# Kernel tuning notes

Measured on AMD Instinct MI355X. Metric: run time of the kernel, lower is better.

The kernel has to match this reference:

```python
import jax, jax.numpy as jnp
import numpy as np

N = 50000
E = 800000
D_IN = 128
D_HID = 512
D_OUT = 128
BN_EPS = 1e-5


def setup_inputs() -> dict:
    key = jax.random.key(0)
    ks = jax.random.split(key, 12)
    inp = {}
    inp["v"] = jax.random.normal(ks[0], (N, D_IN), dtype=jnp.float32)
    inp["src"] = jax.random.randint(ks[1], (E,), 0, N, dtype=jnp.int32)
    inp["dst"] = jax.random.randint(ks[2], (E,), 0, N, dtype=jnp.int32)
    inp["edge_weight"] = jax.random.uniform(ks[3], (E,), dtype=jnp.float32)
    # learned parameters
    inp["epsilon"] = jnp.zeros((1, 1), dtype=jnp.float32)  # nn.Parameter([[0.0]])
    s1 = 1.0 / np.sqrt(D_IN)
    s2 = 1.0 / np.sqrt(D_HID)
    inp["W1"] = jax.random.uniform(ks[4], (D_IN, D_HID), minval=-s1, maxval=s1, dtype=jnp.float32)
    inp["b1"] = jax.random.uniform(ks[5], (D_HID,), minval=-s1, maxval=s1, dtype=jnp.float32)
    inp["gamma1"] = jnp.ones((D_HID,), dtype=jnp.float32)
    inp["beta1"] = jnp.zeros((D_HID,), dtype=jnp.float32)
    inp["W2"] = jax.random.uniform(ks[6], (D_HID, D_OUT), minval=-s2, maxval=s2, dtype=jnp.float32)
    inp["b2"] = jax.random.uniform(ks[7], (D_OUT,), minval=-s2, maxval=s2, dtype=jnp.float32)
    inp["gamma2"] = jnp.ones((D_OUT,), dtype=jnp.float32)
    inp["beta2"] = jnp.zeros((D_OUT,), dtype=jnp.float32)
    return inp


def _batchnorm(x, gamma, beta):
    # training-mode BN: batch mean / biased variance over the node axis
    mean = jnp.mean(x, axis=0)
    var = jnp.mean(jnp.square(x - mean), axis=0)
    return gamma * (x - mean) * jax.lax.rsqrt(var + BN_EPS) + beta


def reference(v, src, dst, edge_weight, epsilon, W1, b1, gamma1, beta1, W2, b2, gamma2, beta2):
    n = v.shape[0]
    # sparse.mm(a, v): out[dst] += w * v[src]
    msgs = v[src] * edge_weight[:, None]               # [E, D_IN]
    v_agg = jax.ops.segment_sum(msgs, dst, num_segments=n)  # [N, D_IN]
    v_agg = v_agg + epsilon * v                        # epsilon residual
    h = jax.nn.relu(_batchnorm(v_agg @ W1 + b1, gamma1, beta1))
    out = jax.nn.relu(_batchnorm(h @ W2 + b2, gamma2, beta2))
    return out
```

## Files before the change

kernel.cpp:

```cpp
#include <hip/hip_runtime.h>

#define N_NODES 50000
#define E_EDGES 800000
#define D_INF   128
#define D_HIDF  512
#define D_OUTF  128
#define SCAN_NB ((N_NODES + 255) / 256)
#define MBLKS   ((N_NODES + 255) / 256)
#define G2BLKS  ((N_NODES + 63) / 64)
#define EQ      (E_EDGES / 4)

typedef unsigned short u16;
typedef __attribute__((ext_vector_type(8))) short short8;
typedef __attribute__((ext_vector_type(4))) float floatx4;

__device__ __forceinline__ u16 f2bf(float f) {
    union { float f; unsigned u; } v; v.f = f;
    unsigned r = (v.u + 0x7fffu + ((v.u >> 16) & 1u)) >> 16;
    return (u16)r;
}
__device__ __forceinline__ float bf2f(u16 b) {
    union { unsigned u; float f; } v; v.u = ((unsigned)b) << 16; return v.f;
}

__global__ void cast_v_kernel(const float* __restrict__ v, u16* __restrict__ vbf) {
    int i = blockIdx.x * blockDim.x + threadIdx.x;
    if (i >= N_NODES * D_INF / 8) return;
    const float4 a = ((const float4*)v)[i * 2];
    const float4 b = ((const float4*)v)[i * 2 + 1];
    u16 o[8];
    o[0] = f2bf(a.x); o[1] = f2bf(a.y); o[2] = f2bf(a.z); o[3] = f2bf(a.w);
    o[4] = f2bf(b.x); o[5] = f2bf(b.y); o[6] = f2bf(b.z); o[7] = f2bf(b.w);
    ((float4*)vbf)[i] = *(const float4*)o;
}

__global__ void hist_kernel(const int* __restrict__ dst, int* __restrict__ counts,
                            int* __restrict__ pos) {
    int t = blockIdx.x * blockDim.x + threadIdx.x;
    if (t >= EQ) return;
    int d0 = dst[t];
    int d1 = dst[t + EQ];
    int d2 = dst[t + 2 * EQ];
    int d3 = dst[t + 3 * EQ];
    int p0 = atomicAdd(&counts[d0], 1);
    int p1 = atomicAdd(&counts[d1], 1);
    int p2 = atomicAdd(&counts[d2], 1);
    int p3 = atomicAdd(&counts[d3], 1);
    pos[t]          = p0;
    pos[t + EQ]     = p1;
    pos[t + 2 * EQ] = p2;
    pos[t + 3 * EQ] = p3;
}

__global__ void prep_w1_kernel(const float* __restrict__ W1, u16* __restrict__ W1t) {
    int idx = blockIdx.x * blockDim.x + threadIdx.x;
    if (idx >= 128 * 512) return;
    int k1 = idx >> 9, n1 = idx & 511;
    W1t[n1 * 128 + k1] = f2bf(W1[idx]);
}

__global__ void prep_w2_kernel(const float* __restrict__ W2, const float* __restrict__ scale1,
                               u16* __restrict__ W2t) {
    int idx = blockIdx.x * blockDim.x + threadIdx.x;
    if (idx >= 512 * 128) return;
    int k2 = idx >> 7, n2 = idx & 127;
    W2t[n2 * 512 + k2] = f2bf(W2[idx] * scale1[k2]);
}

__global__ __launch_bounds__(256) void reduce_kernel(const int* __restrict__ counts,
                                                     int* __restrict__ block_sums) {
    __shared__ int lsum[4];
    int tid = threadIdx.x;
    int gid = blockIdx.x * 256 + tid;
    int s = (gid < N_NODES) ? counts[gid] : 0;
#pragma unroll
    for (int off = 32; off; off >>= 1) s += __shfl_down(s, off);
    if ((tid & 63) == 0) lsum[tid >> 6] = s;
    __syncthreads();
    if (tid == 0) block_sums[blockIdx.x] = lsum[0] + lsum[1] + lsum[2] + lsum[3];
}

__global__ __launch_bounds__(256) void scan_final(const int* __restrict__ counts,
                                                  const int* __restrict__ block_sums,
                                                  int* __restrict__ row_start) {
    __shared__ int sh[256];
    __shared__ int bs[256];
    int tid = threadIdx.x;
    int gid = blockIdx.x * 256 + tid;
    sh[tid] = (gid < N_NODES) ? counts[gid] : 0;
    bs[tid] = (tid < SCAN_NB) ? block_sums[tid] : 0;
    __syncthreads();
    for (int off = 1; off < 256; off <<= 1) {
        int t1 = (tid >= off) ? sh[tid - off] : 0;
        int t2 = (tid >= off) ? bs[tid - off] : 0;
        __syncthreads();
        sh[tid] += t1;
        bs[tid] += t2;
        __syncthreads();
    }
    int boff = (blockIdx.x == 0) ? 0 : bs[blockIdx.x - 1];
    int excl = (tid == 0) ? 0 : sh[tid - 1];
    if (gid < N_NODES) row_start[gid] = boff + excl;
    if (gid == 0) row_start[N_NODES] = E_EDGES;
}

__global__ void fill_kernel(const int* __restrict__ src, const int* __restrict__ dst,
                            const float* __restrict__ w, const int* __restrict__ pos,
                            const int* __restrict__ row_start,
                            int2* __restrict__ csr_ew) {
    int e = blockIdx.x * blockDim.x + threadIdx.x;
    if (e >= E_EDGES) return;
    int d = dst[e];
    int idx = row_start[d] + pos[e];
    int2 rec;
    rec.x = src[e];
    rec.y = __float_as_int(w[e]);
    csr_ew[idx] = rec;
}

__global__ __launch_bounds__(256) void gather_kernel(const u16* __restrict__ vbf,
                                                     const int* __restrict__ row_start,
                                                     const int2* __restrict__ csr_ew,
                                                     const float* __restrict__ eps_p,
                                                     u16* __restrict__ vagg) {
    int node = blockIdx.x * 16 + (threadIdx.x >> 4);
    if (node >= N_NODES) return;
    int c8 = (threadIdx.x & 15) << 3;
    int beg = row_start[node];
    int end = row_start[node + 1];
    float a[8] = {};
    int j = beg;
    for (; j + 1 < end; j += 2) {
        int2 e0 = csr_ew[j];
        int2 e1 = csr_ew[j + 1];
        float w0 = __int_as_float(e0.y);
        float w1 = __int_as_float(e1.y);
        float4 r0 = *(const float4*)(vbf + (size_t)e0.x * D_INF + c8);
        float4 r1 = *(const float4*)(vbf + (size_t)e1.x * D_INF + c8);
        const u16* p0 = (const u16*)&r0;
        const u16* p1 = (const u16*)&r1;
#pragma unroll
        for (int t = 0; t < 8; ++t) a[t] += w0 * bf2f(p0[t]);
#pragma unroll
        for (int t = 0; t < 8; ++t) a[t] += w1 * bf2f(p1[t]);
    }
    if (j < end) {
        int2 e0 = csr_ew[j];
        float w0 = __int_as_float(e0.y);
        float4 r0 = *(const float4*)(vbf + (size_t)e0.x * D_INF + c8);
        const u16* p0 = (const u16*)&r0;
#pragma unroll
        for (int t = 0; t < 8; ++t) a[t] += w0 * bf2f(p0[t]);
    }
    float e = eps_p[0];
    float4 rn = *(const float4*)(vbf + (size_t)node * D_INF + c8);
    const u16* pn = (const u16*)&rn;
    u16 o[8];
#pragma unroll
    for (int t = 0; t < 8; ++t) o[t] = f2bf(a[t] + e * bf2f(pn[t]));
    *(float4*)(vagg + (size_t)node * D_INF + c8) = *(const float4*)o;
}

template<int MT, int NT, int TH, int WRW, int FUSE, int BDIR>
__global__ __launch_bounds__(TH) void mfma_gemm_bn(
        const u16* __restrict__ A, const u16* __restrict__ Bt,
        const float* __restrict__ bias,
        const float* __restrict__ a_shift,
        u16* __restrict__ Cout,
        float* __restrict__ psum, float* __restrict__ psq,
        int M, int Ncols, int K) {
    constexpr int WAVES = TH / 64;
    constexpr int WCW = WAVES / WRW;
    constexpr int WMS = MT / WRW;
    constexpr int WNS = NT / WCW;
    constexpr int MI = WMS / 16;
    constexpr int NJ = WNS / 16;
    constexpr int RP = TH / 4;
    constexpr int RH = MT / RP;
    constexpr int JH = NT / 64;
    constexpr int STG = MT * 80 + (BDIR ? 0 : NT * 80);
    constexpr int OBUF = RP * 68 * 4;
    constexpr int SMEM_BYTES = (STG > OBUF) ? STG : OBUF;
    __shared__ __align__(16) char smem_raw[SMEM_BYTES];
    u16* As = (u16*)smem_raw;
    u16* Bs = As + MT * 40;
    const int bm = blockIdx.y * MT;
    const int bn = blockIdx.x * NT;
    const int tid = threadIdx.x;
    const int wave = tid >> 6, lane = tid & 63;
    const int wr = wave / WCW, wc = wave % WCW;
    const int wm = wr * WMS;
    const int wn = wc * WNS;
    const int lm = lane & 15, quad = lane >> 4;

    floatx4 acc[MI][NJ] = {};

    constexpr int UNITS = (MT + (BDIR ? 0 : NT)) * 4;
    constexpr int NU = UNITS / TH;
    static_assert(NU * TH == UNITS, "staging units must divide thread count");

    const int ksteps = K >> 5;

    float4 areg[NU];
#pragma unroll
    for (int u = 0; u < NU; ++u) {
        int c = tid + u * TH;
        int r = c >> 2, kk = (c & 3) << 3;
        float4 av = make_float4(0.f, 0.f, 0.f, 0.f);
        if (r < MT) {
            int row = bm + r;
            if (row < M) av = *(const float4*)(A + (size_t)row * K + kk);
        } else {
            av = *(const float4*)(Bt + (size_t)(bn + r - MT) * K + kk);
        }
        areg[u] = av;
    }
    short8 bnext[BDIR ? NJ : 1];
    if constexpr (BDIR) {
#pragma unroll
        for (int j = 0; j < NJ; ++j)
            bnext[j] = *(const short8*)(Bt + (size_t)(bn + wn + j * 16 + lm) * K + quad * 8);
    }

    for (int ks = 0; ks < ksteps; ++ks) {
        const int k0 = ks << 5;
#pragma unroll
        for (int u = 0; u < NU; ++u) {
            int c = tid + u * TH;
            int r = c >> 2, kk = (c & 3) << 3;
            float4 av = areg[u];
            if (r < MT) {
                if constexpr (FUSE) {
                    if (bm + r < M) {
                        u16* ab = (u16*)&av;
                        const float4 h0 = *(const float4*)(a_shift + k0 + kk);
                        const float4 h1 = *(const float4*)(a_shift + k0 + kk + 4);
                        ab[0] = f2bf(fmaxf(0.f, bf2f(ab[0]) + h0.x));
                        ab[1] = f2bf(fmaxf(0.f, bf2f(ab[1]) + h0.y));
                        ab[2] = f2bf(fmaxf(0.f, bf2f(ab[2]) + h0.z));
                        ab[3] = f2bf(fmaxf(0.f, bf2f(ab[3]) + h0.w));
                        ab[4] = f2bf(fmaxf(0.f, bf2f(ab[4]) + h1.x));
                        ab[5] = f2bf(fmaxf(0.f, bf2f(ab[5]) + h1.y));
                        ab[6] = f2bf(fmaxf(0.f, bf2f(ab[6]) + h1.z));
                        ab[7] = f2bf(fmaxf(0.f, bf2f(ab[7]) + h1.w));
                    }
                }
                *(float4*)&As[r * 40 + kk] = av;
            } else {
                *(float4*)&Bs[(r - MT) * 40 + kk] = av;
            }
        }
        if (ks + 1 < ksteps) {
            const int k1 = k0 + 32;
#pragma unroll
            for (int u = 0; u < NU; ++u) {
                int c = tid + u * TH;
                int r = c >> 2, kk = (c & 3) << 3;
                float4 av = make_float4(0.f, 0.f, 0.f, 0.f);
                if (r < MT) {
                    int row = bm + r;
                    if (row < M) av = *(const float4*)(A + (size_t)row * K + k1 + kk);
                } else {
                    av = *(const float4*)(Bt + (size_t)(bn + r - MT) * K + k1 + kk);
                }
                areg[u] = av;
            }
        }
        __syncthreads();
        short8 af[MI], bcur[NJ];
#pragma unroll
        for (int i = 0; i < MI; ++i)
            af[i] = *(const short8*)&As[(wm + i * 16 + lm) * 40 + quad * 8];
        if constexpr (BDIR) {
#pragma unroll
            for (int j = 0; j < NJ; ++j) bcur[j] = bnext[j];
            if (ks + 1 < ksteps) {
#pragma unroll
                for (int j = 0; j < NJ; ++j)
                    bnext[j] = *(const short8*)(Bt + (size_t)(bn + wn + j * 16 + lm) * K
                                                + k0 + 32 + quad * 8);
            }
        } else {
#pragma unroll
            for (int j = 0; j < NJ; ++j)
                bcur[j] = *(const short8*)&Bs[(wn + j * 16 + lm) * 40 + quad * 8];
        }
#pragma unroll
        for (int i = 0; i < MI; ++i)
#pragma unroll
            for (int j = 0; j < NJ; ++j)
                acc[i][j] = __builtin_amdgcn_mfma_f32_16x16x32_bf16(af[i], bcur[j], acc[i][j], 0, 0, 0);
        __syncthreads();
    }

    float* redS = (float*)smem_raw;
    float* redQ = redS + NT;
    if (tid < NT) { redS[tid] = 0.f; redQ[tid] = 0.f; }
    __syncthreads();
    float bjv[NJ];
#pragma unroll
    for (int j = 0; j < NJ; ++j) {
        int cl = wn + j * 16 + lm;
        bjv[j] = bias[bn + cl];
        float s = 0.f, q = 0.f;
#pragma unroll
        for (int i = 0; i < MI; ++i) {
            int row0 = bm + wm + i * 16 + quad * 4;
#pragma unroll
            for (int r = 0; r < 4; ++r) {
                if (row0 + r < M) {
                    float x = acc[i][j][r] + bjv[j];
                    s += x; q += x * x;
                }
            }
        }
        s += __shfl_xor(s, 16); q += __shfl_xor(q, 16);
        s += __shfl_xor(s, 32); q += __shfl_xor(q, 32);
        if (quad == 0) {
            atomicAdd(&redS[cl], s);
            atomicAdd(&redQ[cl], q);
        }
    }
    __syncthreads();
    if (tid < NT) {
        psum[(size_t)blockIdx.y * Ncols + bn + tid] = redS[tid];
        psq [(size_t)blockIdx.y * Ncols + bn + tid] = redQ[tid];
    }

    float* obuf = (float*)smem_raw;
#pragma unroll
    for (int rh = 0; rh < RH; ++rh) {
#pragma unroll
        for (int jh = 0; jh < JH; ++jh) {
            __syncthreads();
            bool part = ((wm / RP) == rh) && ((wn >> 6) == jh);
            if (part) {
                int rbase = wm % RP;
#pragma unroll
                for (int i = 0; i < MI; ++i)
#pragma unroll
                    for (int j = 0; j < NJ; ++j) {
                        int cp = (wn & 63) + j * 16 + lm;
#pragma unroll
                        for (int r = 0; r < 4; ++r)
                            obuf[(rbase + i * 16 + quad * 4 + r) * 68 + cp] =
                                acc[i][j][r] + bjv[j];
                    }
            }
            __syncthreads();
            int lr = tid >> 2;
            int seg = (tid & 3) << 4;
            int grow = bm + rh * RP + lr;
            if (grow < M) {
                u16 ob[16];
#pragma unroll
                for (int t = 0; t < 4; ++t) {
                    float4 f = *(float4*)&obuf[lr * 68 + seg + t * 4];
                    ob[t * 4 + 0] = f2bf(f.x);
                    ob[t * 4 + 1] = f2bf(f.y);
                    ob[t * 4 + 2] = f2bf(f.z);
                    ob[t * 4 + 3] = f2bf(f.w);
                }
                u16* dstp = Cout + (size_t)grow * Ncols + bn + jh * 64 + seg;
                *(float4*)dstp       = *(float4*)(ob);
                *(float4*)(dstp + 8) = *(float4*)(ob + 8);
            }
        }
    }
}

__global__ __launch_bounds__(1024) void bn_finalize_kernel(
        const float* __restrict__ psum, const float* __restrict__ psq,
        const float* __restrict__ gamma, const float* __restrict__ beta,
        float* __restrict__ scale, float* __restrict__ shift, float* __restrict__ tshift,
        int nblocks, int Ncols, float inv_n) {
    __shared__ float shS[16][64];
    __shared__ float shQ[16][64];
    const int tx = threadIdx.x;
    const int ty = threadIdx.y;
    const int c = blockIdx.x * 64 + tx;
    float s = 0.f, q = 0.f;
    for (int b = ty; b < nblocks; b += 16) {
        s += psum[(size_t)b * Ncols + c];
        q += psq [(size_t)b * Ncols + c];
    }
    shS[ty][tx] = s;
    shQ[ty][tx] = q;
    __syncthreads();
    if (ty == 0) {
        float S = 0.f, Q = 0.f;
#pragma unroll
        for (int r = 0; r < 16; ++r) { S += shS[r][tx]; Q += shQ[r][tx]; }
        float m = S * inv_n;
        float var = Q * inv_n - m * m;
        float rs = rsqrtf(var + 1e-5f);
        float sc = gamma[c] * rs;
        float sh = beta[c] - sc * m;
        scale[c] = sc;
        shift[c] = sh;
        if (tshift) tshift[c] = sh / sc;
    }
}

__global__ void bn2_apply_kernel(const u16* __restrict__ X, float* __restrict__ Y,
                                 const float* __restrict__ scale,
                                 const float* __restrict__ shift, int n8) {
    int i = blockIdx.x * blockDim.x + threadIdx.x;
    if (i >= n8) return;
    int c = (i & 15) << 3;
    float4 raw = ((const float4*)X)[i];
    const u16* xb = (const u16*)&raw;
    float4 sc0 = *(const float4*)(scale + c);
    float4 sc1 = *(const float4*)(scale + c + 4);
    float4 sh0 = *(const float4*)(shift + c);
    float4 sh1 = *(const float4*)(shift + c + 4);
    float4 y0, y1;
    y0.x = fmaxf(0.f, bf2f(xb[0]) * sc0.x + sh0.x);
    y0.y = fmaxf(0.f, bf2f(xb[1]) * sc0.y + sh0.y);
    y0.z = fmaxf(0.f, bf2f(xb[2]) * sc0.z + sh0.z);
    y0.w = fmaxf(0.f, bf2f(xb[3]) * sc0.w + sh0.w);
    y1.x = fmaxf(0.f, bf2f(xb[4]) * sc1.x + sh1.x);
    y1.y = fmaxf(0.f, bf2f(xb[5]) * sc1.y + sh1.y);
    y1.z = fmaxf(0.f, bf2f(xb[6]) * sc1.z + sh1.z);
    y1.w = fmaxf(0.f, bf2f(xb[7]) * sc1.w + sh1.w);
    ((float4*)Y)[i * 2]     = y0;
    ((float4*)Y)[i * 2 + 1] = y1;
}

extern "C" void kernel_launch(void* const* d_in, const int* in_sizes, int n_in,
                              void* d_out, int out_size, void* d_ws, size_t ws_size,
                              hipStream_t stream) {
    const float* v    = (const float*)d_in[0];
    const int* src    = (const int*)d_in[1];
    const int* dst    = (const int*)d_in[2];
    const float* ew   = (const float*)d_in[3];
    const float* eps  = (const float*)d_in[4];
    const float* W1   = (const float*)d_in[5];
    const float* b1   = (const float*)d_in[6];
    const float* g1   = (const float*)d_in[7];
    const float* be1  = (const float*)d_in[8];
    const float* W2   = (const float*)d_in[9];
    const float* b2   = (const float*)d_in[10];
    const float* g2   = (const float*)d_in[11];
    const float* be2  = (const float*)d_in[12];
    float* out = (float*)d_out;

    char* base = (char*)d_ws;
    u16* x1   = (u16*)(base);
    u16* vbf  = (u16*)(base + 51200000ull);
    u16* vagg = (u16*)(base + 64000000ull);
    u16* x2   = (u16*)(base + 76800000ull);
    u16* W1t  = (u16*)(base + 89600000ull);
    u16* W2t  = (u16*)(base + 89731072ull);
    float* psum   = (float*)(base + 89862144ull);
    float* psq    = (float*)(base + 90663168ull);
    float* scale1 = (float*)(base + 91464192ull);
    float* shift1 = scale1 + 512;
    float* scale2 = shift1 + 512;
    float* shift2 = scale2 + 128;
    float* tshift1 = shift2 + 128;
    int* counts     = (int*)(tshift1 + 512);
    int* row_start  = counts + 50000;
    int* pos        = row_start + 50004;
    int2* csr_ew    = (int2*)(pos + 800000);
    int* block_sums = (int*)(csr_ew + 800000);

    hipMemsetAsync(counts, 0, (size_t)50000 * sizeof(int), stream);

    cast_v_kernel<<<(N_NODES * D_INF / 8 + 255) / 256, 256, 0, stream>>>(v, vbf);
    hist_kernel<<<(EQ + 255) / 256, 256, 0, stream>>>(dst, counts, pos);
    prep_w1_kernel<<<(128 * 512 + 255) / 256, 256, 0, stream>>>(W1, W1t);
    reduce_kernel<<<SCAN_NB, 256, 0, stream>>>(counts, block_sums);
    scan_final<<<SCAN_NB, 256, 0, stream>>>(counts, block_sums, row_start);
    fill_kernel<<<(E_EDGES + 255) / 256, 256, 0, stream>>>(src, dst, ew, pos, row_start, csr_ew);
    gather_kernel<<<(N_NODES + 15) / 16, 256, 0, stream>>>(vbf, row_start, csr_ew, eps, vagg);

    {
        dim3 grid(D_HIDF / 128, MBLKS);
        mfma_gemm_bn<256, 128, 512, 4, 0, 0><<<grid, 512, 0, stream>>>(
            vagg, W1t, b1, nullptr, x1, psum, psq, N_NODES, D_HIDF, D_INF);
    }
    bn_finalize_kernel<<<D_HIDF / 64, dim3(64, 16), 0, stream>>>(
        psum, psq, g1, be1, scale1, shift1, tshift1, MBLKS, D_HIDF, 1.0f / N_NODES);

    prep_w2_kernel<<<(512 * 128 + 255) / 256, 256, 0, stream>>>(W2, scale1, W2t);

    {
        dim3 grid(1, G2BLKS);
        mfma_gemm_bn<64, 128, 256, 1, 1, 1><<<grid, 256, 0, stream>>>(
            x1, W2t, b2, tshift1, x2, psum, psq, N_NODES, D_OUTF, D_HIDF);
    }
    bn_finalize_kernel<<<D_OUTF / 64, dim3(64, 16), 0, stream>>>(
        psum, psq, g2, be2, scale2, shift2, nullptr, G2BLKS, D_OUTF, 1.0f / N_NODES);

    {
        int n8 = N_NODES * D_OUTF / 8;
        bn2_apply_kernel<<<(n8 + 255) / 256, 256, 0, stream>>>(x2, out, scale2, shift2, n8);
    }
}
```

Before: 288.9 us.

## Restructure MFMA GEMM to stage A in large K chunks and read B directly from global

The GEMM kernel now stages the A tile in shared memory in large K chunks (the whole K=128 for GEMM1, two 256-wide chunks for GEMM2) instead of 32-wide steps. B fragments are read straight from global/L2 instead of through shared memory. GEMM1 switches to 64-row tiles spanning all 512 output columns, so vagg is read once per row block rather than four times. GEMM2 moves to 512 threads. This cuts barrier count and redundant A loads, but adds more partial-sum blocks for BN1 (stored in reused CSR scratch) and uncoalesced direct B loads from global.

```diff
diff --git a/kernel.cpp b/kernel.cpp
--- a/kernel.cpp
+++ b/kernel.cpp
@@ -6,7 +6,6 @@
 #define D_HIDF  512
 #define D_OUTF  128
 #define SCAN_NB ((N_NODES + 255) / 256)
-#define MBLKS   ((N_NODES + 255) / 256)
 #define G2BLKS  ((N_NODES + 63) / 64)
 #define EQ      (E_EDGES / 4)
 
@@ -161,147 +160,126 @@
     *(float4*)(vagg + (size_t)node * D_INF + c8) = *(const float4*)o;
 }
 
-template<int MT, int NT, int TH, int WRW, int FUSE, int BDIR>
+template<int MT, int NT, int TH, int KC, int KTOT, int FUSE>
 __global__ __launch_bounds__(TH) void mfma_gemm_bn(
         const u16* __restrict__ A, const u16* __restrict__ Bt,
         const float* __restrict__ bias,
         const float* __restrict__ a_shift,
         u16* __restrict__ Cout,
         float* __restrict__ psum, float* __restrict__ psq,
-        int M, int Ncols, int K) {
-    constexpr int WAVES = TH / 64;
-    constexpr int WCW = WAVES / WRW;
+        int M) {
+    constexpr int WCW = 4;
+    constexpr int WRW = TH / 64 / WCW;
     constexpr int WMS = MT / WRW;
     constexpr int WNS = NT / WCW;
     constexpr int MI = WMS / 16;
     constexpr int NJ = WNS / 16;
-    constexpr int RP = TH / 4;
-    constexpr int RH = MT / RP;
-    constexpr int JH = NT / 64;
-    constexpr int STG = MT * 80 + (BDIR ? 0 : NT * 80);
-    constexpr int OBUF = RP * 68 * 4;
-    constexpr int SMEM_BYTES = (STG > OBUF) ? STG : OBUF;
+    constexpr int STRIDE = KC + 8;
+    constexpr int KSC = KC / 32;
+    constexpr int CHUNKS = KTOT / KC;
+    constexpr int UPR = KC / 8;
+    constexpr int UNITS = MT * UPR;
+    constexpr int NU = UNITS / TH;
+    static_assert(NU * TH == UNITS, "staging units must divide thread count");
+    constexpr int SA = MT * STRIDE * 2;
+    constexpr int SO = MT * 68 * 4;
+    constexpr int SR = NT * 8;
+    constexpr int SMEM_BYTES = SA > SO ? (SA > SR ? SA : SR) : (SO > SR ? SO : SR);
     __shared__ __align__(16) char smem_raw[SMEM_BYTES];
     u16* As = (u16*)smem_raw;
-    u16* Bs = As + MT * 40;
-    const int bm = blockIdx.y * MT;
-    const int bn = blockIdx.x * NT;
+
+    const int bm = blockIdx.x * MT;
     const int tid = threadIdx.x;
     const int wave = tid >> 6, lane = tid & 63;
-    const int wr = wave / WCW, wc = wave % WCW;
+    const int wr = wave >> 2, wc = wave & 3;
     const int wm = wr * WMS;
     const int wn = wc * WNS;
     const int lm = lane & 15, quad = lane >> 4;
 
     floatx4 acc[MI][NJ] = {};
-
-    constexpr int UNITS = (MT + (BDIR ? 0 : NT)) * 4;
-    constexpr int NU = UNITS / TH;
-    static_assert(NU * TH == UNITS, "staging units must divide thread count");
-
-    const int ksteps = K >> 5;
-
     float4 areg[NU];
-#pragma unroll
-    for (int u = 0; u < NU; ++u) {
-        int c = tid + u * TH;
-        int r = c >> 2, kk = (c & 3) << 3;
-        float4 av = make_float4(0.f, 0.f, 0.f, 0.f);
-        if (r < MT) {
-            int row = bm + r;
-            if (row < M) av = *(const float4*)(A + (size_t)row * K + kk);
-        } else {
-            av = *(const float4*)(Bt + (size_t)(bn + r - MT) * K + kk);
-        }
-        areg[u] = av;
-    }
-    short8 bnext[BDIR ? NJ : 1];
-    if constexpr (BDIR) {
-#pragma unroll
-        for (int j = 0; j < NJ; ++j)
-            bnext[j] = *(const short8*)(Bt + (size_t)(bn + wn + j * 16 + lm) * K + quad * 8);
-    }
-
-    for (int ks = 0; ks < ksteps; ++ks) {
-        const int k0 = ks << 5;
+
+    auto load_chunk = [&](int chunk) {
 #pragma unroll
         for (int u = 0; u < NU; ++u) {
             int c = tid + u * TH;
-            int r = c >> 2, kk = (c & 3) << 3;
+            int r = c / UPR;
+            int kk = (c % UPR) * 8;
+            float4 av = make_float4(0.f, 0.f, 0.f, 0.f);
+            int row = bm + r;
+            if (row < M) av = *(const float4*)(A + (size_t)row * KTOT + chunk * KC + kk);
+            areg[u] = av;
+        }
+    };
+    auto write_chunk = [&](int chunk) {
+#pragma unroll
+        for (int u = 0; u < NU; ++u) {
+            int c = tid + u * TH;
+            int r = c / UPR;
+            int kk = (c % UPR) * 8;
             float4 av = areg[u];
-            if (r < MT) {
-                if constexpr (FUSE) {
-                    if (bm + r < M) {
-                        u16* ab = (u16*)&av;
-                        const float4 h0 = *(const float4*)(a_shift + k0 + kk);
-                        const float4 h1 = *(const float4*)(a_shift + k0 + kk + 4);
-                        ab[0] = f2bf(fmaxf(0.f, bf2f(ab[0]) + h0.x));
-                        ab[1] = f2bf(fmaxf(0.f, bf2f(ab[1]) + h0.y));
-                        ab[2] = f2bf(fmaxf(0.f, bf2f(ab[2]) + h0.z));
-                        ab[3] = f2bf(fmaxf(0.f, bf2f(ab[3]) + h0.w));
-                        ab[4] = f2bf(fmaxf(0.f, bf2f(ab[4]) + h1.x));
-                        ab[5] = f2bf(fmaxf(0.f, bf2f(ab[5]) + h1.y));
-                        ab[6] = f2bf(fmaxf(0.f, bf2f(ab[6]) + h1.z));
-                        ab[7] = f2bf(fmaxf(0.f, bf2f(ab[7]) + h1.w));
-                    }
+            if constexpr (FUSE) {
+                if (bm + r < M) {
+                    u16* ab = (u16*)&av;
+                    int ka = chunk * KC + kk;
+                    const float4 h0 = *(const float4*)(a_shift + ka);
+                    const float4 h1 = *(const float4*)(a_shift + ka + 4);
+                    ab[0] = f2bf(fmaxf(0.f, bf2f(ab[0]) + h0.x));
+                    ab[1] = f2bf(fmaxf(0.f, bf2f(ab[1]) + h0.y));
+                    ab[2] = f2bf(fmaxf(0.f, bf2f(ab[2]) + h0.z));
+                    ab[3] = f2bf(fmaxf(0.f, bf2f(ab[3]) + h0.w));
+                    ab[4] = f2bf(fmaxf(0.f, bf2f(ab[4]) + h1.x));
+                    ab[5] = f2bf(fmaxf(0.f, bf2f(ab[5]) + h1.y));
+                    ab[6] = f2bf(fmaxf(0.f, bf2f(ab[6]) + h1.z));
+                    ab[7] = f2bf(fmaxf(0.f, bf2f(ab[7]) + h1.w));
                 }
-                *(float4*)&As[r * 40 + kk] = av;
-            } else {
-                *(float4*)&Bs[(r - MT) * 40 + kk] = av;
             }
-        }
-        if (ks + 1 < ksteps) {
-            const int k1 = k0 + 32;
-#pragma unroll
-            for (int u = 0; u < NU; ++u) {
-                int c = tid + u * TH;
-                int r = c >> 2, kk = (c & 3) << 3;
-                float4 av = make_float4(0.f, 0.f, 0.f, 0.f);
-                if (r < MT) {
-                    int row = bm + r;
-                    if (row < M) av = *(const float4*)(A + (size_t)row * K + k1 + kk);
-                } else {
-                    av = *(const float4*)(Bt + (size_t)(bn + r - MT) * K + k1 + kk);
-                }
-                areg[u] = av;
-            }
-        }
-        __syncthreads();
-        short8 af[MI], bcur[NJ];
-#pragma unroll
-        for (int i = 0; i < MI; ++i)
-            af[i] = *(const short8*)&As[(wm + i * 16 + lm) * 40 + quad * 8];
-        if constexpr (BDIR) {
-#pragma unroll
-            for (int j = 0; j < NJ; ++j) bcur[j] = bnext[j];
-            if (ks + 1 < ksteps) {
+            *(float4*)&As[r * STRIDE + kk] = av;
+        }
+    };
+    auto compute_chunk = [&](int chunk) {
+#pragma unroll
+        for (int ks = 0; ks < KSC; ++ks) {
+            short8 af[MI], bf[NJ];
+#pragma unroll
+            for (int i = 0; i < MI; ++i)
+                af[i] = *(const short8*)&As[(wm + i * 16 + lm) * STRIDE + ks * 32 + quad * 8];
+#pragma unroll
+            for (int j = 0; j < NJ; ++j)
+                bf[j] = *(const short8*)(Bt + (size_t)(wn + j * 16 + lm) * KTOT
+                                         + chunk * KC + ks * 32 + quad * 8);
+#pragma unroll
+            for (int i = 0; i < MI; ++i)
 #pragma unroll
                 for (int j = 0; j < NJ; ++j)
-                    bnext[j] = *(const short8*)(Bt + (size_t)(bn + wn + j * 16 + lm) * K
-                                                + k0 + 32 + quad * 8);
-            }
-        } else {
-#pragma unroll
-            for (int j = 0; j < NJ; ++j)
-                bcur[j] = *(const short8*)&Bs[(wn + j * 16 + lm) * 40 + quad * 8];
-        }
-#pragma unroll
-        for (int i = 0; i < MI; ++i)
-#pragma unroll
-            for (int j = 0; j < NJ; ++j)
-                acc[i][j] = __builtin_amdgcn_mfma_f32_16x16x32_bf16(af[i], bcur[j], acc[i][j], 0, 0, 0);
-        __syncthreads();
-    }
-
+                    acc[i][j] = __builtin_amdgcn_mfma_f32_16x16x32_bf16(af[i], bf[j], acc[i][j], 0, 0, 0);
+        }
+    };
+
+    load_chunk(0);
+    write_chunk(0);
+    if (CHUNKS > 1) load_chunk(1);
+    __syncthreads();
+    compute_chunk(0);
+#pragma unroll
+    for (int ch = 1; ch < CHUNKS; ++ch) {
+        __syncthreads();
+        write_chunk(ch);
+        if (ch + 1 < CHUNKS) load_chunk(ch + 1);
+        __syncthreads();
+        compute_chunk(ch);
+    }
+
+    __syncthreads();
     float* redS = (float*)smem_raw;
     float* redQ = redS + NT;
-    if (tid < NT) { redS[tid] = 0.f; redQ[tid] = 0.f; }
+    for (int c = tid; c < NT; c += TH) { redS[c] = 0.f; redQ[c] = 0.f; }
     __syncthreads();
     float bjv[NJ];
 #pragma unroll
     for (int j = 0; j < NJ; ++j) {
         int cl = wn + j * 16 + lm;
-        bjv[j] = bias[bn + cl];
+        bjv[j] = bias[cl];
         float s = 0.f, q = 0.f;
 #pragma unroll
         for (int i = 0; i < MI; ++i) {
@@ -322,35 +300,33 @@
         }
     }
     __syncthreads();
-    if (tid < NT) {
-        psum[(size_t)blockIdx.y * Ncols + bn + tid] = redS[tid];
-        psq [(size_t)blockIdx.y * Ncols + bn + tid] = redQ[tid];
+    for (int c = tid; c < NT; c += TH) {
+        psum[(size_t)blockIdx.x * NT + c] = redS[c];
+        psq [(size_t)blockIdx.x * NT + c] = redQ[c];
     }
 
     float* obuf = (float*)smem_raw;
 #pragma unroll
-    for (int rh = 0; rh < RH; ++rh) {
-#pragma unroll
-        for (int jh = 0; jh < JH; ++jh) {
-            __syncthreads();
-            bool part = ((wm / RP) == rh) && ((wn >> 6) == jh);
-            if (part) {
-                int rbase = wm % RP;
+    for (int jh = 0; jh < NT / 64; ++jh) {
+        __syncthreads();
+#pragma unroll
+        for (int j = 0; j < NJ; ++j) {
+            int gc = wn + j * 16;
+            if (gc >= jh * 64 && gc < jh * 64 + 64) {
+                int cp = gc - jh * 64 + lm;
 #pragma unroll
                 for (int i = 0; i < MI; ++i)
 #pragma unroll
-                    for (int j = 0; j < NJ; ++j) {
-                        int cp = (wn & 63) + j * 16 + lm;
-#pragma unroll
-                        for (int r = 0; r < 4; ++r)
-                            obuf[(rbase + i * 16 + quad * 4 + r) * 68 + cp] =
-                                acc[i][j][r] + bjv[j];
-                    }
+                    for (int r = 0; r < 4; ++r)
+                        obuf[(wm + i * 16 + quad * 4 + r) * 68 + cp] =
+                            acc[i][j][r] + bjv[j];
             }
-            __syncthreads();
-            int lr = tid >> 2;
-            int seg = (tid & 3) << 4;
-            int grow = bm + rh * RP + lr;
+        }
+        __syncthreads();
+        int lr = tid >> 2;
+        int seg = (tid & 3) << 4;
+        if (lr < MT) {
+            int grow = bm + lr;
             if (grow < M) {
                 u16 ob[16];
 #pragma unroll
@@ -361,7 +337,7 @@
                     ob[t * 4 + 2] = f2bf(f.z);
                     ob[t * 4 + 3] = f2bf(f.w);
                 }
-                u16* dstp = Cout + (size_t)grow * Ncols + bn + jh * 64 + seg;
+                u16* dstp = Cout + (size_t)grow * NT + jh * 64 + seg;
                 *(float4*)dstp       = *(float4*)(ob);
                 *(float4*)(dstp + 8) = *(float4*)(ob + 8);
             }
@@ -452,8 +428,8 @@
     u16* x2   = (u16*)(base + 76800000ull);
     u16* W1t  = (u16*)(base + 89600000ull);
     u16* W2t  = (u16*)(base + 89731072ull);
-    float* psum   = (float*)(base + 89862144ull);
-    float* psq    = (float*)(base + 90663168ull);
+    float* psum2  = (float*)(base + 89862144ull);
+    float* psq2   = (float*)(base + 90663168ull);
     float* scale1 = (float*)(base + 91464192ull);
     float* shift1 = scale1 + 512;
     float* scale2 = shift1 + 512;
@@ -464,6 +440,8 @@
     int* pos        = row_start + 50004;
     int2* csr_ew    = (int2*)(pos + 800000);
     int* block_sums = (int*)(csr_ew + 800000);
+    float* psum1 = (float*)pos;
+    float* psq1  = (float*)csr_ew;
 
     hipMemsetAsync(counts, 0, (size_t)50000 * sizeof(int), stream);
 
@@ -475,23 +453,17 @@
     fill_kernel<<<(E_EDGES + 255) / 256, 256, 0, stream>>>(src, dst, ew, pos, row_start, csr_ew);
     gather_kernel<<<(N_NODES + 15) / 16, 256, 0, stream>>>(vbf, row_start, csr_ew, eps, vagg);
 
-    {
-        dim3 grid(D_HIDF / 128, MBLKS);
-        mfma_gemm_bn<256, 128, 512, 4, 0, 0><<<grid, 512, 0, stream>>>(
-            vagg, W1t, b1, nullptr, x1, psum, psq, N_NODES, D_HIDF, D_INF);
-    }
+    mfma_gemm_bn<64, 512, 512, 128, 128, 0><<<G2BLKS, 512, 0, stream>>>(
+        vagg, W1t, b1, nullptr, x1, psum1, psq1, N_NODES);
     bn_finalize_kernel<<<D_HIDF / 64, dim3(64, 16), 0, stream>>>(
-        psum, psq, g1, be1, scale1, shift1, tshift1, MBLKS, D_HIDF, 1.0f / N_NODES);
+        psum1, psq1, g1, be1, scale1, shift1, tshift1, G2BLKS, D_HIDF, 1.0f / N_NODES);
 
     prep_w2_kernel<<<(512 * 128 + 255) / 256, 256, 0, stream>>>(W2, scale1, W2t);
 
-    {
-        dim3 grid(1, G2BLKS);
-        mfma_gemm_bn<64, 128, 256, 1, 1, 1><<<grid, 256, 0, stream>>>(
-            x1, W2t, b2, tshift1, x2, psum, psq, N_NODES, D_OUTF, D_HIDF);
-    }
+    mfma_gemm_bn<64, 128, 512, 256, 512, 1><<<G2BLKS, 512, 0, stream>>>(
+        x1, W2t, b2, tshift1, x2, psum2, psq2, N_NODES);
     bn_finalize_kernel<<<D_OUTF / 64, dim3(64, 16), 0, stream>>>(
-        psum, psq, g2, be2, scale2, shift2, nullptr, G2BLKS, D_OUTF, 1.0f / N_NODES);
+        psum2, psq2, g2, be2, scale2, shift2, nullptr, G2BLKS, D_OUTF, 1.0f / N_NODES);
 
     {
         int n8 = N_NODES * D_OUTF / 8;
```

After: 352.9 us. 22.2% more time.

## Stage GEMM tiles via direct global-to-LDS loads with XOR swizzle

Applied to the files above, without the earlier changes.

Rewrites the MFMA GEMM+BN kernel so tile staging uses global_load_lds (direct global-to-LDS DMA) with an XOR-swizzled 32-element LDS stride, instead of register-staged loads with padded rows. The second GEMM moves from 64-row/256-thread blocks with B read straight from global into 128-row/512-thread blocks that stage both A (with the fused shift+relu) and B through LDS. The register double-buffering prefetch is removed, so global loads are no longer overlapped with MFMA within a block. Overlap now has to come from occupancy, and the change risks exposed latency.

```diff
diff --git a/kernel.cpp b/kernel.cpp
--- a/kernel.cpp
+++ b/kernel.cpp
@@ -6,13 +6,15 @@
 #define D_HIDF  512
 #define D_OUTF  128
 #define SCAN_NB ((N_NODES + 255) / 256)
-#define MBLKS   ((N_NODES + 255) / 256)
-#define G2BLKS  ((N_NODES + 63) / 64)
+#define M1BLKS  ((N_NODES + 255) / 256)
+#define M2BLKS  ((N_NODES + 127) / 128)
 #define EQ      (E_EDGES / 4)
 
 typedef unsigned short u16;
 typedef __attribute__((ext_vector_type(8))) short short8;
 typedef __attribute__((ext_vector_type(4))) float floatx4;
+typedef const __attribute__((address_space(1))) void gas_t;
+typedef __attribute__((address_space(3))) void las_t;
 
 __device__ __forceinline__ u16 f2bf(float f) {
     union { float f; unsigned u; } v; v.f = f;
@@ -161,80 +163,86 @@
     *(float4*)(vagg + (size_t)node * D_INF + c8) = *(const float4*)o;
 }
 
-template<int MT, int NT, int TH, int WRW, int FUSE, int BDIR>
-__global__ __launch_bounds__(TH) void mfma_gemm_bn(
+template<int MT, int NT, int FUSE, int AGL, int KTOT>
+__global__ __launch_bounds__(512) void mfma_gemm_bn(
         const u16* __restrict__ A, const u16* __restrict__ Bt,
         const float* __restrict__ bias,
         const float* __restrict__ a_shift,
         u16* __restrict__ Cout,
         float* __restrict__ psum, float* __restrict__ psq,
-        int M, int Ncols, int K) {
-    constexpr int WAVES = TH / 64;
-    constexpr int WCW = WAVES / WRW;
-    constexpr int WMS = MT / WRW;
-    constexpr int WNS = NT / WCW;
+        int M, int Ncols) {
+    constexpr int WMS = MT / 4;
+    constexpr int WNS = NT / 2;
+    static_assert(WNS == 64, "col wave span must be 64");
     constexpr int MI = WMS / 16;
     constexpr int NJ = WNS / 16;
-    constexpr int RP = TH / 4;
+    constexpr int ASTR = AGL ? 32 : 48;
+    constexpr int ABYTES = MT * ASTR * 2;
+    constexpr int STG = ABYTES + NT * 64;
+    constexpr int RP = 128;
     constexpr int RH = MT / RP;
     constexpr int JH = NT / 64;
-    constexpr int STG = MT * 80 + (BDIR ? 0 : NT * 80);
-    constexpr int OBUF = RP * 68 * 4;
-    constexpr int SMEM_BYTES = (STG > OBUF) ? STG : OBUF;
-    __shared__ __align__(16) char smem_raw[SMEM_BYTES];
-    u16* As = (u16*)smem_raw;
-    u16* Bs = As + MT * 40;
+    constexpr int OB = RP * 68 * 4;
+    constexpr int SMEM = STG > OB ? STG : OB;
+    __shared__ __align__(16) char smem[SMEM];
+    u16* As = (u16*)smem;
+    u16* Bs = (u16*)(smem + ABYTES);
+
+    constexpr int ACH = AGL ? MT / 16 : 0;
+    constexpr int BCH = NT / 16;
+    constexpr int CPW = (ACH + BCH) / 8;
+    static_assert(CPW * 8 == ACH + BCH, "chunks must divide waves");
+    constexpr int AU = AGL ? 0 : (MT * 4) / 512;
+    static_assert(AGL || AU * 512 == MT * 4, "A units must divide threads");
+
     const int bm = blockIdx.y * MT;
     const int bn = blockIdx.x * NT;
     const int tid = threadIdx.x;
     const int wave = tid >> 6, lane = tid & 63;
-    const int wr = wave / WCW, wc = wave % WCW;
+    const int wr = wave >> 1, wc = wave & 1;
     const int wm = wr * WMS;
     const int wn = wc * WNS;
     const int lm = lane & 15, quad = lane >> 4;
 
     floatx4 acc[MI][NJ] = {};
 
-    constexpr int UNITS = (MT + (BDIR ? 0 : NT)) * 4;
-    constexpr int NU = UNITS / TH;
-    static_assert(NU * TH == UNITS, "staging units must divide thread count");
-
-    const int ksteps = K >> 5;
-
-    float4 areg[NU];
-#pragma unroll
-    for (int u = 0; u < NU; ++u) {
-        int c = tid + u * TH;
-        int r = c >> 2, kk = (c & 3) << 3;
-        float4 av = make_float4(0.f, 0.f, 0.f, 0.f);
-        if (r < MT) {
-            int row = bm + r;
-            if (row < M) av = *(const float4*)(A + (size_t)row * K + kk);
-        } else {
-            av = *(const float4*)(Bt + (size_t)(bn + r - MT) * K + kk);
-        }
-        areg[u] = av;
-    }
-    short8 bnext[BDIR ? NJ : 1];
-    if constexpr (BDIR) {
-#pragma unroll
-        for (int j = 0; j < NJ; ++j)
-            bnext[j] = *(const short8*)(Bt + (size_t)(bn + wn + j * 16 + lm) * K + quad * 8);
-    }
-
+    const int ksteps = KTOT >> 5;
     for (int ks = 0; ks < ksteps; ++ks) {
         const int k0 = ks << 5;
-#pragma unroll
-        for (int u = 0; u < NU; ++u) {
-            int c = tid + u * TH;
-            int r = c >> 2, kk = (c & 3) << 3;
-            float4 av = areg[u];
-            if (r < MT) {
-                if constexpr (FUSE) {
-                    if (bm + r < M) {
+        {
+            const int sub = lane >> 2, s = lane & 3;
+#pragma unroll
+            for (int t = 0; t < CPW; ++t) {
+                int ch = wave * CPW + t;
+                if (AGL && ch < ACH) {
+                    int row = ch * 16 + sub;
+                    int grow = bm + row; if (grow > M - 1) grow = M - 1;
+                    int ss = s ^ (row & 3);
+                    __builtin_amdgcn_global_load_lds(
+                        (gas_t*)(A + (size_t)grow * KTOT + k0 + ss * 8),
+                        (las_t*)(As + row * 32 + s * 8), 16, 0, 0);
+                } else {
+                    int row = (ch - ACH) * 16 + sub;
+                    int ss = s ^ (row & 3);
+                    __builtin_amdgcn_global_load_lds(
+                        (gas_t*)(Bt + (size_t)(bn + row) * KTOT + k0 + ss * 8),
+                        (las_t*)(Bs + row * 32 + s * 8), 16, 0, 0);
+                }
+            }
+        }
+        if constexpr (!AGL) {
+#pragma unroll
+            for (int u = 0; u < AU; ++u) {
+                int c = tid + u * 512;
+                int r = c >> 2, s = c & 3;
+                float4 av = make_float4(0.f, 0.f, 0.f, 0.f);
+                int grow = bm + r;
+                if (grow < M) {
+                    av = *(const float4*)(A + (size_t)grow * KTOT + k0 + s * 8);
+                    if constexpr (FUSE) {
                         u16* ab = (u16*)&av;
-                        const float4 h0 = *(const float4*)(a_shift + k0 + kk);
-                        const float4 h1 = *(const float4*)(a_shift + k0 + kk + 4);
+                        const float4 h0 = *(const float4*)(a_shift + k0 + s * 8);
+                        const float4 h1 = *(const float4*)(a_shift + k0 + s * 8 + 4);
                         ab[0] = f2bf(fmaxf(0.f, bf2f(ab[0]) + h0.x));
                         ab[1] = f2bf(fmaxf(0.f, bf2f(ab[1]) + h0.y));
                         ab[2] = f2bf(fmaxf(0.f, bf2f(ab[2]) + h0.z));
@@ -245,55 +253,33 @@
                         ab[7] = f2bf(fmaxf(0.f, bf2f(ab[7]) + h1.w));
                     }
                 }
-                *(float4*)&As[r * 40 + kk] = av;
-            } else {
-                *(float4*)&Bs[(r - MT) * 40 + kk] = av;
+                *(float4*)&As[r * 48 + s * 8] = av;
             }
         }
-        if (ks + 1 < ksteps) {
-            const int k1 = k0 + 32;
-#pragma unroll
-            for (int u = 0; u < NU; ++u) {
-                int c = tid + u * TH;
-                int r = c >> 2, kk = (c & 3) << 3;
-                float4 av = make_float4(0.f, 0.f, 0.f, 0.f);
-                if (r < MT) {
-                    int row = bm + r;
-                    if (row < M) av = *(const float4*)(A + (size_t)row * K + k1 + kk);
-                } else {
-                    av = *(const float4*)(Bt + (size_t)(bn + r - MT) * K + k1 + kk);
-                }
-                areg[u] = av;
-            }
-        }
         __syncthreads();
-        short8 af[MI], bcur[NJ];
+        short8 af[MI], bfr[NJ];
+#pragma unroll
+        for (int i = 0; i < MI; ++i) {
+            int row = wm + i * 16 + lm;
+            if constexpr (AGL)
+                af[i] = *(const short8*)&As[row * 32 + (quad ^ (row & 3)) * 8];
+            else
+                af[i] = *(const short8*)&As[row * 48 + quad * 8];
+        }
+#pragma unroll
+        for (int j = 0; j < NJ; ++j) {
+            int row = wn + j * 16 + lm;
+            bfr[j] = *(const short8*)&Bs[row * 32 + (quad ^ (row & 3)) * 8];
+        }
 #pragma unroll
         for (int i = 0; i < MI; ++i)
-            af[i] = *(const short8*)&As[(wm + i * 16 + lm) * 40 + quad * 8];
-        if constexpr (BDIR) {
-#pragma unroll
-            for (int j = 0; j < NJ; ++j) bcur[j] = bnext[j];
-            if (ks + 1 < ksteps) {
-#pragma unroll
-                for (int j = 0; j < NJ; ++j)
-                    bnext[j] = *(const short8*)(Bt + (size_t)(bn + wn + j * 16 + lm) * K
-                                                + k0 + 32 + quad * 8);
-            }
-        } else {
 #pragma unroll
             for (int j = 0; j < NJ; ++j)
-                bcur[j] = *(const short8*)&Bs[(wn + j * 16 + lm) * 40 + quad * 8];
-        }
-#pragma unroll
-        for (int i = 0; i < MI; ++i)
-#pragma unroll
-            for (int j = 0; j < NJ; ++j)
-                acc[i][j] = __builtin_amdgcn_mfma_f32_16x16x32_bf16(af[i], bcur[j], acc[i][j], 0, 0, 0);
+                acc[i][j] = __builtin_amdgcn_mfma_f32_16x16x32_bf16(af[i], bfr[j], acc[i][j], 0, 0, 0);
         __syncthreads();
     }
 
-    float* redS = (float*)smem_raw;
+    float* redS = (float*)smem;
     float* redQ = redS + NT;
     if (tid < NT) { redS[tid] = 0.f; redQ[tid] = 0.f; }
     __syncthreads();
@@ -327,20 +313,19 @@
         psq [(size_t)blockIdx.y * Ncols + bn + tid] = redQ[tid];
     }
 
-    float* obuf = (float*)smem_raw;
+    float* obuf = (float*)smem;
 #pragma unroll
     for (int rh = 0; rh < RH; ++rh) {
 #pragma unroll
         for (int jh = 0; jh < JH; ++jh) {
             __syncthreads();
-            bool part = ((wm / RP) == rh) && ((wn >> 6) == jh);
-            if (part) {
+            if ((wm / RP) == rh && (wn >> 6) == jh) {
                 int rbase = wm % RP;
 #pragma unroll
                 for (int i = 0; i < MI; ++i)
 #pragma unroll
                     for (int j = 0; j < NJ; ++j) {
-                        int cp = (wn & 63) + j * 16 + lm;
+                        int cp = j * 16 + lm;
 #pragma unroll
                         for (int r = 0; r < 4; ++r)
                             obuf[(rbase + i * 16 + quad * 4 + r) * 68 + cp] =
@@ -476,22 +461,22 @@
     gather_kernel<<<(N_NODES + 15) / 16, 256, 0, stream>>>(vbf, row_start, csr_ew, eps, vagg);
 
     {
-        dim3 grid(D_HIDF / 128, MBLKS);
-        mfma_gemm_bn<256, 128, 512, 4, 0, 0><<<grid, 512, 0, stream>>>(
-            vagg, W1t, b1, nullptr, x1, psum, psq, N_NODES, D_HIDF, D_INF);
+        dim3 grid(D_HIDF / 128, M1BLKS);
+        mfma_gemm_bn<256, 128, 0, 1, D_INF><<<grid, 512, 0, stream>>>(
+            vagg, W1t, b1, nullptr, x1, psum, psq, N_NODES, D_HIDF);
     }
     bn_finalize_kernel<<<D_HIDF / 64, dim3(64, 16), 0, stream>>>(
-        psum, psq, g1, be1, scale1, shift1, tshift1, MBLKS, D_HIDF, 1.0f / N_NODES);
+        psum, psq, g1, be1, scale1, shift1, tshift1, M1BLKS, D_HIDF, 1.0f / N_NODES);
 
     prep_w2_kernel<<<(512 * 128 + 255) / 256, 256, 0, stream>>>(W2, scale1, W2t);
 
     {
-        dim3 grid(1, G2BLKS);
-        mfma_gemm_bn<64, 128, 256, 1, 1, 1><<<grid, 256, 0, stream>>>(
-            x1, W2t, b2, tshift1, x2, psum, psq, N_NODES, D_OUTF, D_HIDF);
+        dim3 grid(D_OUTF / 128, M2BLKS);
+        mfma_gemm_bn<128, 128, 1, 0, D_HIDF><<<grid, 512, 0, stream>>>(
+            x1, W2t, b2, tshift1, x2, psum, psq, N_NODES, D_OUTF);
     }
     bn_finalize_kernel<<<D_OUTF / 64, dim3(64, 16), 0, stream>>>(
-        psum, psq, g2, be2, scale2, shift2, nullptr, G2BLKS, D_OUTF, 1.0f / N_NODES);
+        psum, psq, g2, be2, scale2, shift2, nullptr, M2BLKS, D_OUTF, 1.0f / N_NODES);
 
     {
         int n8 = N_NODES * D_OUTF / 8;
```

Measured after the change: 281.2 us. 1.03x faster.
